# Performance work log

Measured on AMD Instinct MI355X. Metric: run time of the kernel, lower is better.

## Reference

```python
import jax, jax.numpy as jnp
import numpy as np

B, T, D = 2, 1024, 384
d = D // 3            # 128
D3 = 3 * d            # 384
D9 = 9 * d            # 1152
GAMMA = 5.0
EPS_W = 1e-8
EPS_N = 1e-5


def _orth(rng, n):
    q, _ = np.linalg.qr(rng.standard_normal((n, n)).astype(np.float64))
    return jnp.asarray(q.astype(np.float32))


def setup_inputs() -> dict:
    key = jax.random.key(0)
    x = jax.random.normal(key, (B, T, D), dtype=jnp.float32)
    rng = np.random.default_rng(0)
    def plin(fan_in, fan_out):
        W = jnp.asarray(rng.standard_normal((fan_out, fan_in)).astype(np.float32) * 0.05)
        b = jnp.zeros((fan_out,), jnp.float32)
        return W, b
    Wq, bq = plin(d, D3); Sq = _orth(rng, D3)
    Wk, bk = plin(d, D3); Sk = _orth(rng, D3)
    Wv, bv = plin(d, D3); Sv = _orth(rng, D3)
    Wp, bp = plin(D3, D9)
    gn = jnp.ones((D9,), jnp.float32)
    bn = jnp.zeros((D9,), jnp.float32)
    return {"x": x, "Wq": Wq, "bq": bq, "Sq": Sq, "Wk": Wk, "bk": bk, "Sk": Sk,
            "Wv": Wv, "bv": bv, "Sv": Sv, "Wp": Wp, "bp": bp, "gn": gn, "bn": bn}


def _plin(x, W, b):
    # PositiveLinearHK: linear with softplus-positive weights
    return x @ jax.nn.softplus(W).T + b


def reference(x, Wq, bq, Sq, Wk, bk, Sk, Wv, bv, Sv, Wp, bp, gn, bn):
    Q_base = x[:, :, 0 * d:1 * d]
    K_base = x[:, :, 1 * d:2 * d]
    V_base = x[:, :, 2 * d:3 * d]
    # proj = PositiveLinearHK -> SingleStiefelProjector (orthogonal mixing)
    Q = _plin(Q_base, Wq, bq) @ Sq          # (B,T,3d)
    K = _plin(K_base, Wk, bk) @ Sk
    V = _plin(V_base, Wv, bv) @ Sv
    dots = jnp.einsum('bti,btj->btij', Q, K)            # (B,T,3d,3d)
    scores = jax.nn.sigmoid(GAMMA * dots)
    weights = scores / (scores.sum(axis=-1, keepdims=True) + EPS_W)
    attended = jnp.einsum('btij,btj->bti', weights, V)  # (B,T,3d)
    h = _plin(attended, Wp, bp)                         # (B,T,9d)
    mu = h.mean(axis=-1, keepdims=True)
    var = h.var(axis=-1, keepdims=True)
    return (h - mu) * jax.lax.rsqrt(var + EPS_N) * gn + bn
```

## Files before the change

### kernel.cpp

```cpp
#include <hip/hip_runtime.h>
#include <hip/hip_bf16.h>
#include <math.h>

#define NTOK  2048
#define DD    128
#define DD3   384
#define DD9   1152
#define TB    2
#define GAMMA_F 5.0f
#define LN2_F   0.69314718f

#define OFF_M    0
#define OFF_C    147456
#define OFF_WP2  148608

typedef __attribute__((ext_vector_type(2))) float f32x2;

__device__ __forceinline__ float softplusf(float x) {
    return fmaxf(x, 0.0f) + log1pf(__expf(-fabsf(x)));
}
__device__ __forceinline__ unsigned short f2bf(float f) {
    __hip_bfloat16 h = __float2bfloat16(f);
    return *reinterpret_cast<unsigned short*>(&h);
}

__global__ __launch_bounds__(384) void k_prep(const float* __restrict__ Wq, const float* __restrict__ Wk,
                                              const float* __restrict__ Wv, const float* __restrict__ Wp,
                                              const float* __restrict__ Sq, const float* __restrict__ Sk,
                                              const float* __restrict__ Sv, const float* __restrict__ bq,
                                              const float* __restrict__ bk, const float* __restrict__ bv,
                                              float* __restrict__ ws) {
    __shared__ float sw[DD3];
    int b = blockIdx.x, tid = threadIdx.x;
    if (b < 384) {
        int i = b, m = tid;
        unsigned d0 = f2bf(softplusf(Wp[(0 * DD3 + m) * DD3 + i]) - LN2_F);
        unsigned d1 = f2bf(softplusf(Wp[(1 * DD3 + m) * DD3 + i]) - LN2_F);
        unsigned d2 = f2bf(softplusf(Wp[(2 * DD3 + m) * DD3 + i]) - LN2_F);
        unsigned* base = (unsigned*)(ws + OFF_WP2);
        int idx = (i >> 1) * (DD3 * 4) + m * 4 + (i & 1) * 2;
        uint2 u; u.x = d0 | (d1 << 16); u.y = d2;
        *(uint2*)(base + idx) = u;
    } else if (b < 768) {
        int bb = b - 384;
        int mat = bb >> 7, i = bb & 127;
        const float* W = (mat == 0) ? Wq : (mat == 1 ? Wk : Wv);
        const float* S = (mat == 0) ? Sq : (mat == 1 ? Sk : Sv);
        int m = tid;
        sw[m] = softplusf(W[m * DD + i]);
        __syncthreads();
        const float4* sw4 = (const float4*)sw;
        float a0 = 0.f, a1 = 0.f, a2 = 0.f, a3 = 0.f;
        for (int j4 = 0; j4 < 96; ++j4) {
            float4 w = sw4[j4];
            int j = j4 * 4;
            a0 = fmaf(w.x, S[(j + 0) * DD3 + m], a0);
            a1 = fmaf(w.y, S[(j + 1) * DD3 + m], a1);
            a2 = fmaf(w.z, S[(j + 2) * DD3 + m], a2);
            a3 = fmaf(w.w, S[(j + 3) * DD3 + m], a3);
        }
        ws[OFF_M + mat * 49152 + (i >> 2) * (DD3 * 4) + m * 4 + (i & 3)] = (a0 + a1) + (a2 + a3);
    } else {
        int mat = b - 768;
        const float* S = (mat == 0) ? Sq : (mat == 1 ? Sk : Sv);
        const float* bb_ = (mat == 0) ? bq : (mat == 1 ? bk : bv);
        int m = tid;
        float a0 = 0.f, a1 = 0.f, a2 = 0.f, a3 = 0.f;
        for (int j4 = 0; j4 < 96; ++j4) {
            int j = j4 * 4;
            a0 = fmaf(bb_[j + 0], S[(j + 0) * DD3 + m], a0);
            a1 = fmaf(bb_[j + 1], S[(j + 1) * DD3 + m], a1);
            a2 = fmaf(bb_[j + 2], S[(j + 2) * DD3 + m], a2);
            a3 = fmaf(bb_[j + 3], S[(j + 3) * DD3 + m], a3);
        }
        ws[OFF_C + mat * DD3 + m] = (a0 + a1) + (a2 + a3);
    }
}

#define PSIG(FQ2, K2, V2, RS2, AV2) do {                                      \
        f32x2 x_ = __builtin_elementwise_min(                                  \
                     __builtin_elementwise_max((FQ2) * (K2), NEG1), POS1);     \
        f32x2 w_ = x_ * x_;                                                    \
        f32x2 p_ = __builtin_elementwise_fma(                                  \
                   __builtin_elementwise_fma(                                  \
                   __builtin_elementwise_fma(                                  \
                   __builtin_elementwise_fma(                                  \
                   __builtin_elementwise_fma(                                  \
                   __builtin_elementwise_fma(PC13, w_, PC11),                  \
                     w_, PC9), w_, PC7), w_, PC5), w_, PC3), w_, PC1);         \
        f32x2 s_ = __builtin_elementwise_fma(x_, p_, HALF2);                   \
        RS2 = RS2 + s_;                                                        \
        AV2 = __builtin_elementwise_fma(s_, (V2), AV2);                        \
    } while (0)

__global__ __launch_bounds__(384, 6) void k_fused(const float* __restrict__ x,
                                                  const float* __restrict__ bp,
                                                  const float* __restrict__ gn,
                                                  const float* __restrict__ bn,
                                                  const float* __restrict__ ws,
                                                  float* __restrict__ out) {
    __shared__ float qkv[3 * TB * DD3];
    __shared__ float att[TB * DD3];
    __shared__ float red[16];
    __shared__ float ssum[TB], smu[TB], sinv[TB];

    int tid = threadIdx.x;
    int tok0 = blockIdx.x * TB;
    const float* xb = x + (size_t)tok0 * DD3;

#pragma unroll
    for (int mat = 0; mat < 3; ++mat) {
        const float4* M4 = (const float4*)(ws + OFF_M + mat * 49152);
        const float* xt0 = xb + 0 * DD3 + mat * DD;
        const float* xt1 = xb + 1 * DD3 + mat * DD;
        float a0 = 0.f, a1 = 0.f;
        for (int i4 = 0; i4 < 32; ++i4) {
            float4 mm = M4[i4 * DD3 + tid];
            int i = i4 * 4;
            a0 = fmaf(xt0[i], mm.x, fmaf(xt0[i + 1], mm.y, fmaf(xt0[i + 2], mm.z, fmaf(xt0[i + 3], mm.w, a0))));
            a1 = fmaf(xt1[i], mm.x, fmaf(xt1[i + 1], mm.y, fmaf(xt1[i + 2], mm.z, fmaf(xt1[i + 3], mm.w, a1))));
        }
        float c = ws[OFF_C + mat * DD3 + tid];
        qkv[(mat * TB + 0) * DD3 + tid] = a0 + c;
        qkv[(mat * TB + 1) * DD3 + tid] = a1 + c;
    }
    __syncthreads();

    {
        const f32x2 NEG1  = (f32x2){-1.0f, -1.0f};
        const f32x2 POS1  = (f32x2){ 1.0f,  1.0f};
        const f32x2 HALF2 = (f32x2){ 0.5f,  0.5f};
        const f32x2 PC1   = (f32x2){  1.4919730f,   1.4919730f};
        const f32x2 PC3   = (f32x2){ -4.1350490f,  -4.1350490f};
        const f32x2 PC5   = (f32x2){ 10.9501565f,  10.9501565f};
        const f32x2 PC7   = (f32x2){-20.0847165f, -20.0847165f};
        const f32x2 PC9   = (f32x2){ 22.6396415f,  22.6396415f};
        const f32x2 PC11  = (f32x2){-13.8982400f, -13.8982400f};
        const f32x2 PC13  = (f32x2){  3.5340290f,   3.5340290f};

        int t  = tid / 192;
        int ts = tid - t * 192;
        const float* Qt = qkv + t * DD3;
        float fq0s = Qt[ts]       * (GAMMA_F / 6.0f);
        float fq1s = Qt[ts + 192] * (GAMMA_F / 6.0f);
        f32x2 fq0 = (f32x2){fq0s, fq0s};
        f32x2 fq1 = (f32x2){fq1s, fq1s};
        const float4* K4 = (const float4*)(qkv + (TB + t) * DD3);
        const float4* V4 = (const float4*)(qkv + (2 * TB + t) * DD3);
        f32x2 rs0 = (f32x2){0.f, 0.f}, rs1 = (f32x2){0.f, 0.f};
        f32x2 av0 = (f32x2){0.f, 0.f}, av1 = (f32x2){0.f, 0.f};
        for (int j4 = 0; j4 < 96; ++j4) {
            float4 kk = K4[j4];
            float4 vv = V4[j4];
            f32x2 kxy = (f32x2){kk.x, kk.y}, kzw = (f32x2){kk.z, kk.w};
            f32x2 vxy = (f32x2){vv.x, vv.y}, vzw = (f32x2){vv.z, vv.w};
            PSIG(fq0, kxy, vxy, rs0, av0);
            PSIG(fq0, kzw, vzw, rs0, av0);
            PSIG(fq1, kxy, vxy, rs1, av1);
            PSIG(fq1, kzw, vzw, rs1, av1);
        }
        float rsum0 = rs0.x + rs0.y, rsum1 = rs1.x + rs1.y;
        float avs0  = av0.x + av0.y, avs1  = av1.x + av1.y;
        att[t * DD3 + ts]       = avs0 * __builtin_amdgcn_rcpf(rsum0 + 1e-8f);
        att[t * DD3 + ts + 192] = avs1 * __builtin_amdgcn_rcpf(rsum1 + 1e-8f);
    }
    __syncthreads();

    int wave = tid >> 6, lane64 = tid & 63;

    {
        float s0 = att[0 * DD3 + tid];
        float s1 = att[1 * DD3 + tid];
#pragma unroll
        for (int off = 32; off; off >>= 1) {
            s0 += __shfl_down(s0, off, 64);
            s1 += __shfl_down(s1, off, 64);
        }
        if (lane64 == 0) { red[wave] = s0; red[8 + wave] = s1; }
        __syncthreads();
        if (tid < TB) {
            float a = 0.f;
            for (int w = 0; w < 6; ++w) a += red[tid * 8 + w];
            ssum[tid] = a;
        }
        __syncthreads();
    }

    const uint4* wp4 = (const uint4*)(ws + OFF_WP2);
    f32x2 acc2[3];
    {
        float bp0 = bp[tid], bp1 = bp[tid + DD3], bp2 = bp[tid + 2 * DD3];
        float b0 = LN2_F * ssum[0], b1 = LN2_F * ssum[1];
        acc2[0] = (f32x2){bp0 + b0, bp0 + b1};
        acc2[1] = (f32x2){bp1 + b0, bp1 + b1};
        acc2[2] = (f32x2){bp2 + b0, bp2 + b1};
    }
    const float4* att4 = (const float4*)att;
    for (int i4 = 0; i4 < 96; ++i4) {
        float4 a0 = att4[0 * 96 + i4];
        float4 a1 = att4[1 * 96 + i4];
        const float* af0 = (const float*)&a0;
        const float* af1 = (const float*)&a1;
#pragma unroll
        for (int e2 = 0; e2 < 2; ++e2) {
            uint4 u = wp4[(i4 * 2 + e2) * DD3 + tid];
            {
                float w0 = __uint_as_float(u.x << 16);
                float w1 = __uint_as_float(u.x & 0xffff0000u);
                float w2 = __uint_as_float(u.y << 16);
                f32x2 a01 = (f32x2){af0[e2 * 2], af1[e2 * 2]};
                acc2[0] = __builtin_elementwise_fma(a01, (f32x2){w0, w0}, acc2[0]);
                acc2[1] = __builtin_elementwise_fma(a01, (f32x2){w1, w1}, acc2[1]);
                acc2[2] = __builtin_elementwise_fma(a01, (f32x2){w2, w2}, acc2[2]);
            }
            {
                float w0 = __uint_as_float(u.z << 16);
                float w1 = __uint_as_float(u.z & 0xffff0000u);
                float w2 = __uint_as_float(u.w << 16);
                f32x2 a01 = (f32x2){af0[e2 * 2 + 1], af1[e2 * 2 + 1]};
                acc2[0] = __builtin_elementwise_fma(a01, (f32x2){w0, w0}, acc2[0]);
                acc2[1] = __builtin_elementwise_fma(a01, (f32x2){w1, w1}, acc2[1]);
                acc2[2] = __builtin_elementwise_fma(a01, (f32x2){w2, w2}, acc2[2]);
            }
        }
    }
    float av_[3][TB] = {{acc2[0].x, acc2[0].y}, {acc2[1].x, acc2[1].y}, {acc2[2].x, acc2[2].y}};

#pragma unroll
    for (int t = 0; t < TB; ++t) {
        float s = av_[0][t] + av_[1][t] + av_[2][t];
#pragma unroll
        for (int off = 32; off; off >>= 1) s += __shfl_down(s, off, 64);
        if (lane64 == 0) red[t * 8 + wave] = s;
    }
    __syncthreads();
    if (tid < TB) {
        float a = 0.f;
        for (int w = 0; w < 6; ++w) a += red[tid * 8 + w];
        smu[tid] = a * (1.0f / 1152.0f);
    }
    __syncthreads();
#pragma unroll
    for (int t = 0; t < TB; ++t) {
        float mu = smu[t];
        av_[0][t] -= mu; av_[1][t] -= mu; av_[2][t] -= mu;
        float s = fmaf(av_[0][t], av_[0][t], fmaf(av_[1][t], av_[1][t], av_[2][t] * av_[2][t]));
#pragma unroll
        for (int off = 32; off; off >>= 1) s += __shfl_down(s, off, 64);
        if (lane64 == 0) red[t * 8 + wave] = s;
    }
    __syncthreads();
    if (tid < TB) {
        float b = 0.f;
        for (int w = 0; w < 6; ++w) b += red[tid * 8 + w];
        sinv[tid] = __builtin_amdgcn_rsqf(b * (1.0f / 1152.0f) + 1e-5f);
    }
    __syncthreads();
    float g0 = gn[tid], g1 = gn[tid + DD3], g2 = gn[tid + 2 * DD3];
    float b0 = bn[tid], b1 = bn[tid + DD3], b2 = bn[tid + 2 * DD3];
#pragma unroll
    for (int t = 0; t < TB; ++t) {
        float inv = sinv[t];
        size_t base = (size_t)(tok0 + t) * DD9;
        out[base + tid]           = fmaf(av_[0][t] * inv, g0, b0);
        out[base + tid + DD3]     = fmaf(av_[1][t] * inv, g1, b1);
        out[base + tid + 2 * DD3] = fmaf(av_[2][t] * inv, g2, b2);
    }
}

extern "C" void kernel_launch(void* const* d_in, const int* in_sizes, int n_in,
                              void* d_out, int out_size, void* d_ws, size_t ws_size,
                              hipStream_t stream) {
    const float* x  = (const float*)d_in[0];
    const float* Wq = (const float*)d_in[1];
    const float* bq = (const float*)d_in[2];
    const float* Sq = (const float*)d_in[3];
    const float* Wk = (const float*)d_in[4];
    const float* bk = (const float*)d_in[5];
    const float* Sk = (const float*)d_in[6];
    const float* Wv = (const float*)d_in[7];
    const float* bv = (const float*)d_in[8];
    const float* Sv = (const float*)d_in[9];
    const float* Wp = (const float*)d_in[10];
    const float* bp = (const float*)d_in[11];
    const float* gn = (const float*)d_in[12];
    const float* bn = (const float*)d_in[13];
    float* out = (float*)d_out;
    float* ws  = (float*)d_ws;

    hipLaunchKernelGGL(k_prep, dim3(771), dim3(384), 0, stream,
                       Wq, Wk, Wv, Wp, Sq, Sk, Sv, bq, bk, bv, ws);
    hipLaunchKernelGGL(k_fused, dim3(NTOK / TB), dim3(384), 0, stream, x, bp, gn, bn, ws, out);
}
```

Before: 156.3 us.

## Split output projection into separate MFMA bf16 kernel with LayerNorm

The fused kernel is split in two. The attention kernel now writes bf16 attended vectors and their row sums to workspace. A new projection kernel processes 8 tokens per block and does the 384->1152 projection with bf16 16x16x32 MFMA instructions instead of scalar FMAs over bf16-packed weights, then applies bias, the LN2 correction and LayerNorm. This targets the scalar projection cost, but adds a global round-trip for the attention output, an extra launch, and padding of the 8 token rows up to 16 for the MFMA (half the rows are zero).

```diff
diff --git a/kernel.cpp b/kernel.cpp
--- a/kernel.cpp
+++ b/kernel.cpp
@@ -7,14 +7,19 @@
 #define DD3   384
 #define DD9   1152
 #define TB    2
+#define TBP   8
 #define GAMMA_F 5.0f
 #define LN2_F   0.69314718f
 
 #define OFF_M    0
 #define OFF_C    147456
-#define OFF_WP2  148608
+#define OFF_BP   148608
+#define OFF_ATT  369792
+#define OFF_SSUM 763008
 
 typedef __attribute__((ext_vector_type(2))) float f32x2;
+typedef __attribute__((ext_vector_type(8))) short bf16x8;
+typedef __attribute__((ext_vector_type(4))) float f32x4;
 
 __device__ __forceinline__ float softplusf(float x) {
     return fmaxf(x, 0.0f) + log1pf(__expf(-fabsf(x)));
@@ -22,6 +27,9 @@
 __device__ __forceinline__ unsigned short f2bf(float f) {
     __hip_bfloat16 h = __float2bfloat16(f);
     return *reinterpret_cast<unsigned short*>(&h);
+}
+__device__ __forceinline__ float bf2f(unsigned short u) {
+    return __uint_as_float(((unsigned)u) << 16);
 }
 
 __global__ __launch_bounds__(384) void k_prep(const float* __restrict__ Wq, const float* __restrict__ Wk,
@@ -32,17 +40,13 @@
                                               float* __restrict__ ws) {
     __shared__ float sw[DD3];
     int b = blockIdx.x, tid = threadIdx.x;
-    if (b < 384) {
-        int i = b, m = tid;
-        unsigned d0 = f2bf(softplusf(Wp[(0 * DD3 + m) * DD3 + i]) - LN2_F);
-        unsigned d1 = f2bf(softplusf(Wp[(1 * DD3 + m) * DD3 + i]) - LN2_F);
-        unsigned d2 = f2bf(softplusf(Wp[(2 * DD3 + m) * DD3 + i]) - LN2_F);
-        unsigned* base = (unsigned*)(ws + OFF_WP2);
-        int idx = (i >> 1) * (DD3 * 4) + m * 4 + (i & 1) * 2;
-        uint2 u; u.x = d0 | (d1 << 16); u.y = d2;
-        *(uint2*)(base + idx) = u;
-    } else if (b < 768) {
-        int bb = b - 384;
+    if (b < 576) {
+        int idx = b * 384 + tid;
+        unsigned lo = f2bf(softplusf(Wp[2 * idx + 0]) - LN2_F);
+        unsigned hi = f2bf(softplusf(Wp[2 * idx + 1]) - LN2_F);
+        ((unsigned*)(ws + OFF_BP))[idx] = lo | (hi << 16);
+    } else if (b < 960) {
+        int bb = b - 576;
         int mat = bb >> 7, i = bb & 127;
         const float* W = (mat == 0) ? Wq : (mat == 1 ? Wk : Wv);
         const float* S = (mat == 0) ? Sq : (mat == 1 ? Sk : Sv);
@@ -61,7 +65,7 @@
         }
         ws[OFF_M + mat * 49152 + (i >> 2) * (DD3 * 4) + m * 4 + (i & 3)] = (a0 + a1) + (a2 + a3);
     } else {
-        int mat = b - 768;
+        int mat = b - 960;
         const float* S = (mat == 0) ? Sq : (mat == 1 ? Sk : Sv);
         const float* bb_ = (mat == 0) ? bq : (mat == 1 ? bk : bv);
         int m = tid;
@@ -93,16 +97,11 @@
         AV2 = __builtin_elementwise_fma(s_, (V2), AV2);                        \
     } while (0)
 
-__global__ __launch_bounds__(384, 6) void k_fused(const float* __restrict__ x,
-                                                  const float* __restrict__ bp,
-                                                  const float* __restrict__ gn,
-                                                  const float* __restrict__ bn,
-                                                  const float* __restrict__ ws,
-                                                  float* __restrict__ out) {
+__global__ __launch_bounds__(384, 6) void k_attn(const float* __restrict__ x,
+                                                 float* __restrict__ ws) {
     __shared__ float qkv[3 * TB * DD3];
     __shared__ float att[TB * DD3];
     __shared__ float red[16];
-    __shared__ float ssum[TB], smu[TB], sinv[TB];
 
     int tid = threadIdx.x;
     int tok0 = blockIdx.x * TB;
@@ -159,98 +158,126 @@
             PSIG(fq1, kxy, vxy, rs1, av1);
             PSIG(fq1, kzw, vzw, rs1, av1);
         }
-        float rsum0 = rs0.x + rs0.y, rsum1 = rs1.x + rs1.y;
-        float avs0  = av0.x + av0.y, avs1  = av1.x + av1.y;
-        att[t * DD3 + ts]       = avs0 * __builtin_amdgcn_rcpf(rsum0 + 1e-8f);
-        att[t * DD3 + ts + 192] = avs1 * __builtin_amdgcn_rcpf(rsum1 + 1e-8f);
+        float a0 = (av0.x + av0.y) * __builtin_amdgcn_rcpf(rs0.x + rs0.y + 1e-8f);
+        float a1 = (av1.x + av1.y) * __builtin_amdgcn_rcpf(rs1.x + rs1.y + 1e-8f);
+        unsigned short b0 = f2bf(a0), b1 = f2bf(a1);
+        att[t * DD3 + ts]       = bf2f(b0);
+        att[t * DD3 + ts + 192] = bf2f(b1);
+        unsigned short* ag = (unsigned short*)(ws + OFF_ATT);
+        ag[(size_t)(tok0 + t) * DD3 + ts]       = b0;
+        ag[(size_t)(tok0 + t) * DD3 + ts + 192] = b1;
     }
     __syncthreads();
 
     int wave = tid >> 6, lane64 = tid & 63;
-
-    {
-        float s0 = att[0 * DD3 + tid];
-        float s1 = att[1 * DD3 + tid];
-#pragma unroll
-        for (int off = 32; off; off >>= 1) {
-            s0 += __shfl_down(s0, off, 64);
-            s1 += __shfl_down(s1, off, 64);
-        }
-        if (lane64 == 0) { red[wave] = s0; red[8 + wave] = s1; }
-        __syncthreads();
-        if (tid < TB) {
-            float a = 0.f;
-            for (int w = 0; w < 6; ++w) a += red[tid * 8 + w];
-            ssum[tid] = a;
-        }
-        __syncthreads();
-    }
-
-    const uint4* wp4 = (const uint4*)(ws + OFF_WP2);
-    f32x2 acc2[3];
-    {
-        float bp0 = bp[tid], bp1 = bp[tid + DD3], bp2 = bp[tid + 2 * DD3];
-        float b0 = LN2_F * ssum[0], b1 = LN2_F * ssum[1];
-        acc2[0] = (f32x2){bp0 + b0, bp0 + b1};
-        acc2[1] = (f32x2){bp1 + b0, bp1 + b1};
-        acc2[2] = (f32x2){bp2 + b0, bp2 + b1};
-    }
-    const float4* att4 = (const float4*)att;
-    for (int i4 = 0; i4 < 96; ++i4) {
-        float4 a0 = att4[0 * 96 + i4];
-        float4 a1 = att4[1 * 96 + i4];
-        const float* af0 = (const float*)&a0;
-        const float* af1 = (const float*)&a1;
-#pragma unroll
-        for (int e2 = 0; e2 < 2; ++e2) {
-            uint4 u = wp4[(i4 * 2 + e2) * DD3 + tid];
-            {
-                float w0 = __uint_as_float(u.x << 16);
-                float w1 = __uint_as_float(u.x & 0xffff0000u);
-                float w2 = __uint_as_float(u.y << 16);
-                f32x2 a01 = (f32x2){af0[e2 * 2], af1[e2 * 2]};
-                acc2[0] = __builtin_elementwise_fma(a01, (f32x2){w0, w0}, acc2[0]);
-                acc2[1] = __builtin_elementwise_fma(a01, (f32x2){w1, w1}, acc2[1]);
-                acc2[2] = __builtin_elementwise_fma(a01, (f32x2){w2, w2}, acc2[2]);
-            }
-            {
-                float w0 = __uint_as_float(u.z << 16);
-                float w1 = __uint_as_float(u.z & 0xffff0000u);
-                float w2 = __uint_as_float(u.w << 16);
-                f32x2 a01 = (f32x2){af0[e2 * 2 + 1], af1[e2 * 2 + 1]};
-                acc2[0] = __builtin_elementwise_fma(a01, (f32x2){w0, w0}, acc2[0]);
-                acc2[1] = __builtin_elementwise_fma(a01, (f32x2){w1, w1}, acc2[1]);
-                acc2[2] = __builtin_elementwise_fma(a01, (f32x2){w2, w2}, acc2[2]);
-            }
-        }
-    }
-    float av_[3][TB] = {{acc2[0].x, acc2[0].y}, {acc2[1].x, acc2[1].y}, {acc2[2].x, acc2[2].y}};
-
-#pragma unroll
-    for (int t = 0; t < TB; ++t) {
-        float s = av_[0][t] + av_[1][t] + av_[2][t];
-#pragma unroll
-        for (int off = 32; off; off >>= 1) s += __shfl_down(s, off, 64);
-        if (lane64 == 0) red[t * 8 + wave] = s;
-    }
+    float s0 = att[0 * DD3 + tid];
+    float s1 = att[1 * DD3 + tid];
+#pragma unroll
+    for (int off = 32; off; off >>= 1) {
+        s0 += __shfl_down(s0, off, 64);
+        s1 += __shfl_down(s1, off, 64);
+    }
+    if (lane64 == 0) { red[wave] = s0; red[8 + wave] = s1; }
     __syncthreads();
     if (tid < TB) {
         float a = 0.f;
         for (int w = 0; w < 6; ++w) a += red[tid * 8 + w];
-        smu[tid] = a * (1.0f / 1152.0f);
-    }
-    __syncthreads();
-#pragma unroll
-    for (int t = 0; t < TB; ++t) {
-        float mu = smu[t];
-        av_[0][t] -= mu; av_[1][t] -= mu; av_[2][t] -= mu;
-        float s = fmaf(av_[0][t], av_[0][t], fmaf(av_[1][t], av_[1][t], av_[2][t] * av_[2][t]));
+        ws[OFF_SSUM + tok0 + tid] = a;
+    }
+}
+
+__global__ __launch_bounds__(384) void k_proj(const float* __restrict__ bp,
+                                              const float* __restrict__ gn,
+                                              const float* __restrict__ bn,
+                                              const float* __restrict__ ws,
+                                              float* __restrict__ out) {
+    __shared__ unsigned short attb[16 * 392];
+    __shared__ float h[TBP * DD9];
+    __shared__ float red[64];
+    __shared__ float smu[TBP], sinv[TBP];
+
+    int tid = threadIdx.x;
+    int wave = tid >> 6, lane64 = tid & 63;
+    int tok0 = blockIdx.x * TBP;
+
+    {
+        const unsigned short* ag = (const unsigned short*)(ws + OFF_ATT) + (size_t)tok0 * DD3;
+        int r = tid / 48, c = (tid - r * 48) * 8;
+        *(uint4*)(attb + r * 392 + c) = *(const uint4*)(ag + tid * 8);
+        uint4 z; z.x = z.y = z.z = z.w = 0u;
+        *(uint4*)(attb + (8 + r) * 392 + c) = z;
+    }
+    __syncthreads();
+
+    {
+        int n0w  = wave * 192;
+        int brow = lane64 & 15;
+        int koff = (lane64 >> 4) * 8;
+        const unsigned short* Bp = (const unsigned short*)(ws + OFF_BP);
+        const unsigned short* abase = attb + brow * 392 + koff;
+        const unsigned short* bbase = Bp + (size_t)(n0w + brow) * DD3 + koff;
+        f32x4 acc[12];
+#pragma unroll
+        for (int nt = 0; nt < 12; ++nt) acc[nt] = (f32x4){0.f, 0.f, 0.f, 0.f};
+        for (int ks = 0; ks < 12; ++ks) {
+            bf16x8 a = *(const bf16x8*)(abase + ks * 32);
+            const unsigned short* bk_ = bbase + ks * 32;
+#pragma unroll
+            for (int nt = 0; nt < 12; ++nt) {
+                bf16x8 bfr = *(const bf16x8*)(bk_ + nt * 16 * DD3);
+                acc[nt] = __builtin_amdgcn_mfma_f32_16x16x32_bf16(a, bfr, acc[nt], 0, 0, 0);
+            }
+        }
+        if (lane64 < 32) {
+            int rbase = (lane64 >> 4) * 4;
+            int col0  = n0w + (lane64 & 15);
+#pragma unroll
+            for (int nt = 0; nt < 12; ++nt) {
+#pragma unroll
+                for (int r = 0; r < 4; ++r)
+                    h[(rbase + r) * DD9 + col0 + nt * 16] = acc[nt][r];
+            }
+        }
+    }
+    __syncthreads();
+
+    const float* ssums = ws + OFF_SSUM + tok0;
+    float acc3[3][TBP];
+    {
+        float bp0 = bp[tid], bp1 = bp[tid + DD3], bp2 = bp[tid + 2 * DD3];
+#pragma unroll
+        for (int t = 0; t < TBP; ++t) {
+            float base = LN2_F * ssums[t];
+            acc3[0][t] = h[t * DD9 + tid]           + bp0 + base;
+            acc3[1][t] = h[t * DD9 + tid + DD3]     + bp1 + base;
+            acc3[2][t] = h[t * DD9 + tid + 2 * DD3] + bp2 + base;
+        }
+    }
+#pragma unroll
+    for (int t = 0; t < TBP; ++t) {
+        float s = acc3[0][t] + acc3[1][t] + acc3[2][t];
 #pragma unroll
         for (int off = 32; off; off >>= 1) s += __shfl_down(s, off, 64);
         if (lane64 == 0) red[t * 8 + wave] = s;
     }
     __syncthreads();
-    if (tid < TB) {
+    if (tid < TBP) {
+        float a = 0.f;
+        for (int w = 0; w < 6; ++w) a += red[tid * 8 + w];
+        smu[tid] = a * (1.0f / 1152.0f);
+    }
+    __syncthreads();
+#pragma unroll
+    for (int t = 0; t < TBP; ++t) {
+        float mu = smu[t];
+        acc3[0][t] -= mu; acc3[1][t] -= mu; acc3[2][t] -= mu;
+        float s = fmaf(acc3[0][t], acc3[0][t], fmaf(acc3[1][t], acc3[1][t], acc3[2][t] * acc3[2][t]));
+#pragma unroll
+        for (int off = 32; off; off >>= 1) s += __shfl_down(s, off, 64);
+        if (lane64 == 0) red[t * 8 + wave] = s;
+    }
+    __syncthreads();
+    if (tid < TBP) {
         float b = 0.f;
         for (int w = 0; w < 6; ++w) b += red[tid * 8 + w];
         sinv[tid] = __builtin_amdgcn_rsqf(b * (1.0f / 1152.0f) + 1e-5f);
@@ -259,12 +286,12 @@
     float g0 = gn[tid], g1 = gn[tid + DD3], g2 = gn[tid + 2 * DD3];
     float b0 = bn[tid], b1 = bn[tid + DD3], b2 = bn[tid + 2 * DD3];
 #pragma unroll
-    for (int t = 0; t < TB; ++t) {
+    for (int t = 0; t < TBP; ++t) {
         float inv = sinv[t];
         size_t base = (size_t)(tok0 + t) * DD9;
-        out[base + tid]           = fmaf(av_[0][t] * inv, g0, b0);
-        out[base + tid + DD3]     = fmaf(av_[1][t] * inv, g1, b1);
-        out[base + tid + 2 * DD3] = fmaf(av_[2][t] * inv, g2, b2);
+        out[base + tid]           = fmaf(acc3[0][t] * inv, g0, b0);
+        out[base + tid + DD3]     = fmaf(acc3[1][t] * inv, g1, b1);
+        out[base + tid + 2 * DD3] = fmaf(acc3[2][t] * inv, g2, b2);
     }
 }
 
@@ -288,7 +315,8 @@
     float* out = (float*)d_out;
     float* ws  = (float*)d_ws;
 
-    hipLaunchKernelGGL(k_prep, dim3(771), dim3(384), 0, stream,
+    hipLaunchKernelGGL(k_prep, dim3(963), dim3(384), 0, stream,
                        Wq, Wk, Wv, Wp, Sq, Sk, Sv, bq, bk, bv, ws);
-    hipLaunchKernelGGL(k_fused, dim3(NTOK / TB), dim3(384), 0, stream, x, bp, gn, bn, ws, out);
-}
+    hipLaunchKernelGGL(k_attn, dim3(NTOK / TB), dim3(384), 0, stream, x, ws);
+    hipLaunchKernelGGL(k_proj, dim3(NTOK / TBP), dim3(384), 0, stream, bp, gn, bn, ws, out);
+}
```

New measurement: 148.5 us. 5.0% less time.
